# Optimization experiments

Hardware: AMD Instinct MI355X
Metric: run time of the kernel (lower is better)

Reference implementation:

```python
import jax, jax.numpy as jnp
import numpy as np

EPS = 1e-5  # torch LayerNorm default

def setup_inputs() -> dict:
    key = jax.random.key(0)
    k1, k2, k3 = jax.random.split(key, 3)
    x = jax.random.normal(k1, (8, 256, 256, 256), dtype=jnp.float32)
    w_size = 256
    bound = 1.0 / np.sqrt(w_size)
    W = jax.random.uniform(k2, (w_size, w_size), dtype=jnp.float32, minval=-bound, maxval=bound)
    b = jax.random.uniform(k3, (w_size,), dtype=jnp.float32, minval=-bound, maxval=bound)
    return {"x": x, "W": W, "b": b}

def reference(x, W, b):
    # x: [B, 2C, G, Wd]; chunk along channel dim
    u, v = jnp.split(x, 2, axis=1)
    # LayerNorm over all non-batch dims (weight=1, bias=0 since module is
    # constructed fresh inside forward)
    mean = jnp.mean(v, axis=(1, 2, 3), keepdims=True)
    var = jnp.mean(jnp.square(v - mean), axis=(1, 2, 3), keepdims=True)
    v = (v - mean) * jax.lax.rsqrt(var + EPS)
    # Linear along last dim: y = v @ W.T + b
    v = jnp.einsum('bcgw,ow->bcgo', v, W) + b
    return u * (v + 1.0)
```

## Files before the change

kernel.cpp:

```cpp
#include <hip/hip_runtime.h>
#include <hip/hip_bf16.h>

typedef __attribute__((ext_vector_type(8))) short short8_t;
typedef __attribute__((ext_vector_type(4))) float f32x4;

__device__ __forceinline__ short f2bf(float f) {
    union { float f; unsigned u; } v; v.f = f;
    unsigned r = (v.u + 0x7FFFu + ((v.u >> 16) & 1u)) >> 16;
    return (short)r;
}

__device__ __forceinline__ f32x4 ntload4(const float* p) {
    return __builtin_nontemporal_load(reinterpret_cast<const f32x4*>(p));
}
__device__ __forceinline__ void ntstore4(float* p, f32x4 v) {
    __builtin_nontemporal_store(v, reinterpret_cast<f32x4*>(p));
}

#define N_PER_BATCH 8388608.0f
#define LDR 264

__global__ __launch_bounds__(256) void stats_partial(const float* __restrict__ x,
                                                     float2* __restrict__ partials) {
    int bid = blockIdx.x;
    int batch = bid >> 8;
    int blk   = bid & 255;
    const float* base = x + ((size_t)batch << 24) + (1u << 23) + ((size_t)blk << 15);
    int tid = threadIdx.x;
    float s1 = 0.f, s2 = 0.f;
    #pragma unroll
    for (int i = 0; i < 32; ++i) {
        float4 v = *reinterpret_cast<const float4*>(base + (size_t)(i * 256 + tid) * 4);
        s1 += v.x + v.y + v.z + v.w;
        s2 += v.x * v.x + v.y * v.y + v.z * v.z + v.w * v.w;
    }
    #pragma unroll
    for (int off = 32; off; off >>= 1) {
        s1 += __shfl_down(s1, off);
        s2 += __shfl_down(s2, off);
    }
    __shared__ float2 red[4];
    if ((tid & 63) == 0) red[tid >> 6] = make_float2(s1, s2);
    __syncthreads();
    if (tid == 0) {
        float a1 = 0.f, a2 = 0.f;
        #pragma unroll
        for (int w = 0; w < 4; ++w) { a1 += red[w].x; a2 += red[w].y; }
        partials[bid] = make_float2(a1, a2);
    }
}

__global__ __launch_bounds__(1024, 4) void fused_gemm(const float* __restrict__ x,
                                                      const float* __restrict__ W,
                                                      const float* __restrict__ bias,
                                                      const float2* __restrict__ partials,
                                                      float* __restrict__ out) {
    __shared__ short vt[2][16 * LDR];
    __shared__ float2 red2[16];
    __shared__ float2 bst[8];
    const int tid  = threadIdx.x;
    const int wid  = tid >> 6;
    const int lane = tid & 63;
    const int l15  = lane & 15;
    const int l4   = lane >> 4;
    const int q    = l15 & 3;
    const int qg   = l15 >> 2;

    {
        const int bb   = wid >> 1;
        const int half = wid & 1;
        const int li   = ((half << 6) + lane) << 1;
        float2 p0 = partials[(bb << 8) + li];
        float2 p1 = partials[(bb << 8) + li + 1];
        float s1 = p0.x + p1.x, s2 = p0.y + p1.y;
        #pragma unroll
        for (int off = 32; off; off >>= 1) {
            s1 += __shfl_down(s1, off);
            s2 += __shfl_down(s2, off);
        }
        if (lane == 0) red2[wid] = make_float2(s1, s2);
        __syncthreads();
        if (tid < 8) {
            float a1 = red2[2 * tid].x + red2[2 * tid + 1].x;
            float a2 = red2[2 * tid].y + red2[2 * tid + 1].y;
            float mean = a1 / N_PER_BATCH;
            float var  = a2 / N_PER_BATCH - mean * mean;
            bst[tid] = make_float2(mean, rsqrtf(var + 1e-5f));
        }
    }

    short8_t bfrag[8];
    {
        const float* wbase = W + (size_t)(wid * 16 + l15) * 256 + (l4 << 3);
        #pragma unroll
        for (int kb = 0; kb < 8; ++kb) {
            float4 p0 = *reinterpret_cast<const float4*>(wbase + kb * 32);
            float4 p1 = *reinterpret_cast<const float4*>(wbase + kb * 32 + 4);
            short8_t s;
            s[0] = f2bf(p0.x); s[1] = f2bf(p0.y); s[2] = f2bf(p0.z); s[3] = f2bf(p0.w);
            s[4] = f2bf(p1.x); s[5] = f2bf(p1.y); s[6] = f2bf(p1.z); s[7] = f2bf(p1.w);
            bfrag[kb] = s;
        }
    }
    float4 bq = *reinterpret_cast<const float4*>(bias + wid * 16 + (qg << 2));
    bq.x += 1.f; bq.y += 1.f; bq.z += 1.f; bq.w += 1.f;

    const int   srow = tid >> 6;
    const int   scol = (tid & 63) << 2;
    const size_t goff = (size_t)srow * 256 + scol;
    const int   ldsw = srow * LDR + scol;

    const size_t eoff = (size_t)(l4 * 4 + q) * 256 + wid * 16 + (qg << 2);

    const int aoff = l15 * LDR + (l4 << 3);

    const int b = blockIdx.x;
    #define TILE(s) (16383 - (b + ((s) << 8)))
    #define VADDR(T) (x + ((size_t)((T) >> 11) << 24) + (1u << 23) + ((size_t)((T) & 2047) << 12))
    #define UADDR(T) (x + ((size_t)((T) >> 11) << 24) + ((size_t)((T) & 2047) << 12))

    __syncthreads();

    {
        const int T0 = TILE(0);
        const float2 ms0 = bst[T0 >> 11];
        float4 v0 = *reinterpret_cast<const float4*>(VADDR(T0) + goff);
        short4 s;
        s.x = f2bf((v0.x - ms0.x) * ms0.y); s.y = f2bf((v0.y - ms0.x) * ms0.y);
        s.z = f2bf((v0.z - ms0.x) * ms0.y); s.w = f2bf((v0.w - ms0.x) * ms0.y);
        *reinterpret_cast<short4*>(&vt[0][ldsw]) = s;
    }
    float4 vA = *reinterpret_cast<const float4*>(VADDR(TILE(1)) + goff);
    f32x4 uA = ntload4(UADDR(TILE(0)) + eoff);
    f32x4 uB = ntload4(UADDR(TILE(1)) + eoff);
    asm volatile("s_waitcnt lgkmcnt(0)" ::: "memory");
    __builtin_amdgcn_s_barrier();

    for (int s = 0; s < 64; ++s) {
        const int cur = s & 1;
        const int sp1 = (s + 1 < 64) ? s + 1 : 63;
        const int sp2 = (s + 2 < 64) ? s + 2 : 63;
        const int Ts  = TILE(s);
        const int Ts1 = TILE(sp1);
        const int Ts2 = TILE(sp2);

        float4 vB = *reinterpret_cast<const float4*>(VADDR(Ts2) + goff);
        f32x4 uC = ntload4(UADDR(Ts2) + eoff);
        const float2 ms1 = bst[Ts1 >> 11];

        f32x4 acc = {0.f, 0.f, 0.f, 0.f};
        #pragma unroll
        for (int kb = 0; kb < 8; ++kb) {
            short8_t a = *reinterpret_cast<const short8_t*>(&vt[cur][aoff + kb * 32]);
            acc = __builtin_amdgcn_mfma_f32_16x16x32_bf16(a, bfrag[kb], acc, 0, 0, 0);
        }

        float a0 = acc[0], a1 = acc[1], a2 = acc[2], a3 = acc[3];
        float s0 = __shfl_xor(a1, 1), s1v = __shfl_xor(a0, 1);
        float s2v = __shfl_xor(a3, 1), s3 = __shfl_xor(a2, 1);
        const bool qb0 = (q & 1);
        float w0 = qb0 ? s0 : a0;
        float w1 = qb0 ? a1 : s1v;
        float w2 = qb0 ? s2v : a2;
        float w3 = qb0 ? a3 : s3;
        float t0 = __shfl_xor(w2, 2), t1v = __shfl_xor(w3, 2);
        float t2v = __shfl_xor(w0, 2), t3 = __shfl_xor(w1, 2);
        const bool qb1 = (q & 2);
        float x0 = qb1 ? t0 : w0;
        float x1 = qb1 ? t1v : w1;
        float x2 = qb1 ? w2 : t2v;
        float x3 = qb1 ? w3 : t3;

        f32x4 o;
        o[0] = uA[0] * (x0 + bq.x);
        o[1] = uA[1] * (x1 + bq.y);
        o[2] = uA[2] * (x2 + bq.z);
        o[3] = uA[3] * (x3 + bq.w);
        ntstore4(out + ((size_t)Ts << 12) + eoff, o);

        short4 sn;
        sn.x = f2bf((vA.x - ms1.x) * ms1.y); sn.y = f2bf((vA.y - ms1.x) * ms1.y);
        sn.z = f2bf((vA.z - ms1.x) * ms1.y); sn.w = f2bf((vA.w - ms1.x) * ms1.y);
        *reinterpret_cast<short4*>(&vt[cur ^ 1][ldsw]) = sn;

        asm volatile("s_waitcnt lgkmcnt(0)" ::: "memory");
        __builtin_amdgcn_s_barrier();

        vA = vB; uA = uB; uB = uC;
    }
    #undef TILE
    #undef VADDR
    #undef UADDR
}

extern "C" void kernel_launch(void* const* d_in, const int* in_sizes, int n_in,
                              void* d_out, int out_size, void* d_ws, size_t ws_size,
                              hipStream_t stream) {
    const float* x    = (const float*)d_in[0];
    const float* W    = (const float*)d_in[1];
    const float* bias = (const float*)d_in[2];
    float* out = (float*)d_out;

    float2* partials = (float2*)d_ws;

    stats_partial<<<2048, 256, 0, stream>>>(x, partials);
    fused_gemm<<<256, 1024, 0, stream>>>(x, W, bias, partials, out);
}
```

Baseline: 184.7 us.

## Fold LayerNorm stats into GEMM pass and apply normalization algebraically afterward

Replaces the separate stats pass with a GEMM kernel that multiplies raw v by W and accumulates the sum and sum of squares in the same pass. The product is written to workspace as a bf16 intermediate. A second kernel then applies the normalization through the identity rstd*(vW^T) - rstd*mean*rowsum(W), adds the bias and gates with u. The second kernel walks the tiles in reverse order, apparently so the most recently written intermediate is still in cache when it is read back. This removes one full read of v but adds a 128MB intermediate write and read. The new path also rounds the unnormalized product to bf16 and subtracts the mean term afterward, which could lose accuracy if the mean were large. It only runs when the workspace is large enough, otherwise the old path is used.

```diff
diff --git a/kernel.cpp b/kernel.cpp
--- a/kernel.cpp
+++ b/kernel.cpp
@@ -9,6 +9,10 @@
     unsigned r = (v.u + 0x7FFFu + ((v.u >> 16) & 1u)) >> 16;
     return (short)r;
 }
+__device__ __forceinline__ float bf2f(short h) {
+    union { float f; unsigned u; } c; c.u = ((unsigned)(unsigned short)h) << 16;
+    return c.f;
+}
 
 __device__ __forceinline__ f32x4 ntload4(const float* p) {
     return __builtin_nontemporal_load(reinterpret_cast<const f32x4*>(p));
@@ -19,6 +23,217 @@
 
 #define N_PER_BATCH 8388608.0f
 #define LDR 264
+#define TILE(s) (16383 - (b + ((s) << 8)))
+#define VADDR(T) (x + ((size_t)((T) >> 11) << 24) + (1u << 23) + ((size_t)((T) & 2047) << 12))
+#define UADDR(T) (x + ((size_t)((T) >> 11) << 24) + ((size_t)((T) & 2047) << 12))
+
+__global__ __launch_bounds__(1024, 4) void gemm_stats(const float* __restrict__ x,
+                                                      const float* __restrict__ W,
+                                                      short* __restrict__ G,
+                                                      float2* __restrict__ partials) {
+    __shared__ short vt[2][16 * LDR];
+    __shared__ float2 red2w[16];
+    const int tid  = threadIdx.x;
+    const int wid  = tid >> 6;
+    const int lane = tid & 63;
+    const int l15  = lane & 15;
+    const int l4   = lane >> 4;
+    const int q    = l15 & 3;
+    const int qg   = l15 >> 2;
+
+    short8_t bfrag[8];
+    {
+        const float* wbase = W + (size_t)(wid * 16 + l15) * 256 + (l4 << 3);
+        #pragma unroll
+        for (int kb = 0; kb < 8; ++kb) {
+            float4 p0 = *reinterpret_cast<const float4*>(wbase + kb * 32);
+            float4 p1 = *reinterpret_cast<const float4*>(wbase + kb * 32 + 4);
+            short8_t s;
+            s[0] = f2bf(p0.x); s[1] = f2bf(p0.y); s[2] = f2bf(p0.z); s[3] = f2bf(p0.w);
+            s[4] = f2bf(p1.x); s[5] = f2bf(p1.y); s[6] = f2bf(p1.z); s[7] = f2bf(p1.w);
+            bfrag[kb] = s;
+        }
+    }
+
+    const int   srow = tid >> 6;
+    const int   scol = (tid & 63) << 2;
+    const size_t goff = (size_t)srow * 256 + scol;
+    const int   ldsw = srow * LDR + scol;
+    const int   aoff = l15 * LDR + (l4 << 3);
+    const int b = blockIdx.x;
+
+    f32x4 v0 = ntload4(VADDR(TILE(0)) + goff);
+    f32x4 vA = ntload4(VADDR(TILE(1)) + goff);
+    {
+        short4 si;
+        si.x = f2bf(v0[0]); si.y = f2bf(v0[1]); si.z = f2bf(v0[2]); si.w = f2bf(v0[3]);
+        *reinterpret_cast<short4*>(&vt[0][ldsw]) = si;
+    }
+    float accS = v0[0] + v0[1] + v0[2] + v0[3];
+    float accQ = v0[0]*v0[0] + v0[1]*v0[1] + v0[2]*v0[2] + v0[3]*v0[3];
+    __syncthreads();
+
+    for (int s = 0; s < 64; ++s) {
+        const int cur = s & 1;
+        const int sp1 = (s + 1 < 64) ? s + 1 : 63;
+        const int sp2 = (s + 2 < 64) ? s + 2 : 63;
+        const int Ts  = TILE(s);
+        const int Ts2 = TILE(sp2);
+
+        f32x4 vB = ntload4(VADDR(Ts2) + goff);
+
+        if ((s & 7) == 7 && wid == 0 && lane < 16) {
+            float2 pr = red2w[lane];
+            float r1 = pr.x, r2 = pr.y;
+            r1 += __shfl_xor(r1, 8);  r2 += __shfl_xor(r2, 8);
+            r1 += __shfl_xor(r1, 4);  r2 += __shfl_xor(r2, 4);
+            r1 += __shfl_xor(r1, 2);  r2 += __shfl_xor(r2, 2);
+            r1 += __shfl_xor(r1, 1);  r2 += __shfl_xor(r2, 1);
+            if (lane == 0) partials[(7 - (s >> 3)) * 256 + b] = make_float2(r1, r2);
+        }
+
+        f32x4 acc = {0.f, 0.f, 0.f, 0.f};
+        #pragma unroll
+        for (int kb = 0; kb < 8; ++kb) {
+            short8_t a = *reinterpret_cast<const short8_t*>(&vt[cur][aoff + kb * 32]);
+            acc = __builtin_amdgcn_mfma_f32_16x16x32_bf16(a, bfrag[kb], acc, 0, 0, 0);
+        }
+
+        float a0 = acc[0], a1 = acc[1], a2 = acc[2], a3 = acc[3];
+        float e0 = __shfl_xor(a1, 1), e1 = __shfl_xor(a0, 1);
+        float e2 = __shfl_xor(a3, 1), e3 = __shfl_xor(a2, 1);
+        const bool qb0 = (q & 1);
+        float w0 = qb0 ? e0 : a0;
+        float w1 = qb0 ? a1 : e1;
+        float w2 = qb0 ? e2 : a2;
+        float w3 = qb0 ? a3 : e3;
+        float t0 = __shfl_xor(w2, 2), t1 = __shfl_xor(w3, 2);
+        float t2 = __shfl_xor(w0, 2), t3 = __shfl_xor(w1, 2);
+        const bool qb1 = (q & 2);
+        float x0 = qb1 ? t0 : w0;
+        float x1 = qb1 ? t1 : w1;
+        float x2 = qb1 ? w2 : t2;
+        float x3 = qb1 ? w3 : t3;
+
+        short4 g4;
+        g4.x = f2bf(x0); g4.y = f2bf(x1); g4.z = f2bf(x2); g4.w = f2bf(x3);
+        *reinterpret_cast<short4*>(G + ((size_t)Ts << 12) + (tid << 2)) = g4;
+
+        short4 sn;
+        sn.x = f2bf(vA[0]); sn.y = f2bf(vA[1]); sn.z = f2bf(vA[2]); sn.w = f2bf(vA[3]);
+        *reinterpret_cast<short4*>(&vt[cur ^ 1][ldsw]) = sn;
+        if (s < 63) {
+            accS += vA[0] + vA[1] + vA[2] + vA[3];
+            accQ += vA[0]*vA[0] + vA[1]*vA[1] + vA[2]*vA[2] + vA[3]*vA[3];
+        }
+        if ((s & 7) == 6) {
+            float r1 = accS, r2 = accQ;
+            r1 += __shfl_xor(r1, 32); r2 += __shfl_xor(r2, 32);
+            r1 += __shfl_xor(r1, 16); r2 += __shfl_xor(r2, 16);
+            r1 += __shfl_xor(r1, 8);  r2 += __shfl_xor(r2, 8);
+            r1 += __shfl_xor(r1, 4);  r2 += __shfl_xor(r2, 4);
+            r1 += __shfl_xor(r1, 2);  r2 += __shfl_xor(r2, 2);
+            r1 += __shfl_xor(r1, 1);  r2 += __shfl_xor(r2, 1);
+            if (lane == 0) red2w[wid] = make_float2(r1, r2);
+            accS = 0.f; accQ = 0.f;
+        }
+
+        asm volatile("s_waitcnt lgkmcnt(0)" ::: "memory");
+        __builtin_amdgcn_s_barrier();
+        vA = vB;
+    }
+}
+
+__global__ __launch_bounds__(1024) void apply_gate(const float* __restrict__ x,
+                                                   const float* __restrict__ W,
+                                                   const float* __restrict__ bias,
+                                                   const short* __restrict__ G,
+                                                   const float2* __restrict__ partials,
+                                                   float* __restrict__ out) {
+    __shared__ float2 red2[16];
+    __shared__ float2 bst[8];
+    __shared__ float rwacc[1024];
+    __shared__ float cK[2048];
+    const int tid  = threadIdx.x;
+    const int wid  = tid >> 6;
+    const int lane = tid & 63;
+    const int l15  = lane & 15;
+    const int l4   = lane >> 4;
+    const int q    = l15 & 3;
+    const int qg   = l15 >> 2;
+
+    {
+        const float* wb = W + ((size_t)(tid >> 2) << 8) + ((tid & 3) << 6);
+        float rs = 0.f;
+        #pragma unroll
+        for (int i = 0; i < 16; ++i) {
+            float4 w4 = *reinterpret_cast<const float4*>(wb + (i << 2));
+            rs += w4.x + w4.y + w4.z + w4.w;
+        }
+        rwacc[tid] = rs;
+    }
+    {
+        const int bb   = wid >> 1;
+        const int half = wid & 1;
+        const int li   = ((half << 6) + lane) << 1;
+        float2 p0 = partials[(bb << 8) + li];
+        float2 p1 = partials[(bb << 8) + li + 1];
+        float s1 = p0.x + p1.x, s2 = p0.y + p1.y;
+        #pragma unroll
+        for (int off = 32; off; off >>= 1) {
+            s1 += __shfl_down(s1, off);
+            s2 += __shfl_down(s2, off);
+        }
+        if (lane == 0) red2[wid] = make_float2(s1, s2);
+    }
+    __syncthreads();
+    if (tid < 8) {
+        float a1 = red2[2 * tid].x + red2[2 * tid + 1].x;
+        float a2 = red2[2 * tid].y + red2[2 * tid + 1].y;
+        float mean = a1 / N_PER_BATCH;
+        float var  = a2 / N_PER_BATCH - mean * mean;
+        bst[tid] = make_float2(mean, rsqrtf(var + 1e-5f));
+    }
+    __syncthreads();
+    #pragma unroll
+    for (int i = 0; i < 2; ++i) {
+        int idx = tid + (i << 10);
+        int bb = idx >> 8, col = idx & 255;
+        float rs = rwacc[col << 2] + rwacc[(col << 2) + 1]
+                 + rwacc[(col << 2) + 2] + rwacc[(col << 2) + 3];
+        cK[idx] = bias[col] + 1.f - bst[bb].y * bst[bb].x * rs;
+    }
+    __syncthreads();
+
+    const int b = blockIdx.x;
+    const size_t eoff = (size_t)(l4 * 4 + q) * 256 + wid * 16 + (qg << 2);
+    const int col0 = wid * 16 + (qg << 2);
+
+    short4 gA = *reinterpret_cast<const short4*>(G + ((size_t)TILE(63) << 12) + (tid << 2));
+    f32x4  uA = ntload4(UADDR(TILE(63)) + eoff);
+    short4 gB = *reinterpret_cast<const short4*>(G + ((size_t)TILE(62) << 12) + (tid << 2));
+    f32x4  uB = ntload4(UADDR(TILE(62)) + eoff);
+
+    for (int s = 63; s >= 0; --s) {
+        const int sp = (s >= 2) ? s - 2 : 0;
+        const int Ts = TILE(s), Tp = TILE(sp);
+        short4 gC = *reinterpret_cast<const short4*>(G + ((size_t)Tp << 12) + (tid << 2));
+        f32x4  uC = ntload4(UADDR(Tp) + eoff);
+
+        const int bb = Ts >> 11;
+        const float rstd = bst[bb].y;
+        const float4 ck4 = *reinterpret_cast<const float4*>(&cK[(bb << 8) + col0]);
+
+        f32x4 o;
+        o[0] = uA[0] * (rstd * bf2f(gA.x) + ck4.x);
+        o[1] = uA[1] * (rstd * bf2f(gA.y) + ck4.y);
+        o[2] = uA[2] * (rstd * bf2f(gA.z) + ck4.z);
+        o[3] = uA[3] * (rstd * bf2f(gA.w) + ck4.w);
+        ntstore4(out + ((size_t)Ts << 12) + eoff, o);
+
+        gA = gB; gB = gC; uA = uB; uB = uC;
+    }
+}
 
 __global__ __launch_bounds__(256) void stats_partial(const float* __restrict__ x,
                                                      float2* __restrict__ partials) {
@@ -46,7 +261,7 @@
         float a1 = 0.f, a2 = 0.f;
         #pragma unroll
         for (int w = 0; w < 4; ++w) { a1 += red[w].x; a2 += red[w].y; }
-        partials[bid] = make_float2(a1, a2);
+        partials[(batch << 8) + blk] = make_float2(a1, a2);
     }
 }
 
@@ -109,15 +324,9 @@
     const int   scol = (tid & 63) << 2;
     const size_t goff = (size_t)srow * 256 + scol;
     const int   ldsw = srow * LDR + scol;
-
     const size_t eoff = (size_t)(l4 * 4 + q) * 256 + wid * 16 + (qg << 2);
-
-    const int aoff = l15 * LDR + (l4 << 3);
-
+    const int   aoff = l15 * LDR + (l4 << 3);
     const int b = blockIdx.x;
-    #define TILE(s) (16383 - (b + ((s) << 8)))
-    #define VADDR(T) (x + ((size_t)((T) >> 11) << 24) + (1u << 23) + ((size_t)((T) & 2047) << 12))
-    #define UADDR(T) (x + ((size_t)((T) >> 11) << 24) + ((size_t)((T) & 2047) << 12))
 
     __syncthreads();
 
@@ -125,10 +334,10 @@
         const int T0 = TILE(0);
         const float2 ms0 = bst[T0 >> 11];
         float4 v0 = *reinterpret_cast<const float4*>(VADDR(T0) + goff);
-        short4 s;
-        s.x = f2bf((v0.x - ms0.x) * ms0.y); s.y = f2bf((v0.y - ms0.x) * ms0.y);
-        s.z = f2bf((v0.z - ms0.x) * ms0.y); s.w = f2bf((v0.w - ms0.x) * ms0.y);
-        *reinterpret_cast<short4*>(&vt[0][ldsw]) = s;
+        short4 si;
+        si.x = f2bf((v0.x - ms0.x) * ms0.y); si.y = f2bf((v0.y - ms0.x) * ms0.y);
+        si.z = f2bf((v0.z - ms0.x) * ms0.y); si.w = f2bf((v0.w - ms0.x) * ms0.y);
+        *reinterpret_cast<short4*>(&vt[0][ldsw]) = si;
     }
     float4 vA = *reinterpret_cast<const float4*>(VADDR(TILE(1)) + goff);
     f32x4 uA = ntload4(UADDR(TILE(0)) + eoff);
@@ -156,13 +365,13 @@
         }
 
         float a0 = acc[0], a1 = acc[1], a2 = acc[2], a3 = acc[3];
-        float s0 = __shfl_xor(a1, 1), s1v = __shfl_xor(a0, 1);
-        float s2v = __shfl_xor(a3, 1), s3 = __shfl_xor(a2, 1);
+        float e0 = __shfl_xor(a1, 1), e1 = __shfl_xor(a0, 1);
+        float e2 = __shfl_xor(a3, 1), e3 = __shfl_xor(a2, 1);
         const bool qb0 = (q & 1);
-        float w0 = qb0 ? s0 : a0;
-        float w1 = qb0 ? a1 : s1v;
-        float w2 = qb0 ? s2v : a2;
-        float w3 = qb0 ? a3 : s3;
+        float w0 = qb0 ? e0 : a0;
+        float w1 = qb0 ? a1 : e1;
+        float w2 = qb0 ? e2 : a2;
+        float w3 = qb0 ? a3 : e3;
         float t0 = __shfl_xor(w2, 2), t1v = __shfl_xor(w3, 2);
         float t2v = __shfl_xor(w0, 2), t3 = __shfl_xor(w1, 2);
         const bool qb1 = (q & 2);
@@ -188,9 +397,6 @@
 
         vA = vB; uA = uB; uB = uC;
     }
-    #undef TILE
-    #undef VADDR
-    #undef UADDR
 }
 
 extern "C" void kernel_launch(void* const* d_in, const int* in_sizes, int n_in,
@@ -201,8 +407,15 @@
     const float* bias = (const float*)d_in[2];
     float* out = (float*)d_out;
 
-    float2* partials = (float2*)d_ws;
-
-    stats_partial<<<2048, 256, 0, stream>>>(x, partials);
-    fused_gemm<<<256, 1024, 0, stream>>>(x, W, bias, partials, out);
-}
+    const size_t G_BYTES = 134217728ull;
+    if (ws_size >= G_BYTES + 16384) {
+        short*  G        = (short*)d_ws;
+        float2* partials = (float2*)((char*)d_ws + G_BYTES);
+        gemm_stats<<<256, 1024, 0, stream>>>(x, W, G, partials);
+        apply_gate<<<256, 1024, 0, stream>>>(x, W, bias, G, partials, out);
+    } else {
+        float2* partials = (float2*)d_ws;
+        stats_partial<<<2048, 256, 0, stream>>>(x, partials);
+        fused_gemm<<<256, 1024, 0, stream>>>(x, W, bias, partials, out);
+    }
+}
```

New measurement: 248.7 us. +34.6%, slower.
